# Performance work log

Hardware: AMD Instinct MI355X
Metric: run time of the kernel (lower is better)

Reference implementation:

```python
import jax, jax.numpy as jnp
import numpy as np

N = 100000  # nodes
E = 1600000  # edges
D_IN, D_HID, D_OUT = 128, 128, 64
NEG_SLOPE = 0.2


def gat_conv(x, src, dst, W_src, W_dst, att_src, att_dst, bias, num_nodes):
    # PyG GATConv, heads=1, add_self_loops=False.
    h_src = x @ W_src          # [N, C]
    h_dst = x @ W_dst          # [N, C]
    a_src = (h_src * att_src).sum(-1)   # [N]
    a_dst = (h_dst * att_dst).sum(-1)   # [N]
    logits = jax.nn.leaky_relu(a_src[src] + a_dst[dst], NEG_SLOPE)  # [E]
    # segment softmax over destination neighborhoods
    seg_max = jax.ops.segment_max(logits, dst, num_segments=num_nodes)  # [N]
    e = jnp.exp(logits - seg_max[dst])
    denom = jax.ops.segment_sum(e, dst, num_segments=num_nodes)         # [N]
    alpha = e / (denom[dst] + 1e-16)                                    # [E]
    out = jax.ops.segment_sum(alpha[:, None] * h_src[src], dst, num_segments=num_nodes)  # [N, C]
    return out + bias


def setup_inputs() -> dict:
    key = jax.random.key(0)
    ks = jax.random.split(key, 12)
    x = jax.random.normal(ks[0], (N, D_IN), dtype=jnp.float32)
    edge_index = jax.random.randint(ks[1], (2, E), 0, N, dtype=jnp.int64)
    s1 = 1.0 / np.sqrt(D_IN)
    s2 = 1.0 / np.sqrt(D_HID)
    return {
        "x": x,
        "edge_index": edge_index,
        "W1_src": jax.random.uniform(ks[2], (D_IN, D_HID), jnp.float32, -s1, s1),
        "W1_dst": jax.random.uniform(ks[3], (D_IN, D_HID), jnp.float32, -s1, s1),
        "att1_src": jax.random.uniform(ks[4], (D_HID,), jnp.float32, -s2, s2),
        "att1_dst": jax.random.uniform(ks[5], (D_HID,), jnp.float32, -s2, s2),
        "b1": jnp.zeros((D_HID,), jnp.float32),
        "W2_src": jax.random.uniform(ks[6], (D_HID, D_OUT), jnp.float32, -s2, s2),
        "W2_dst": jax.random.uniform(ks[7], (D_HID, D_OUT), jnp.float32, -s2, s2),
        "att2_src": jax.random.uniform(ks[8], (D_OUT,), jnp.float32, -1.0 / np.sqrt(D_OUT), 1.0 / np.sqrt(D_OUT)),
        "att2_dst": jax.random.uniform(ks[9], (D_OUT,), jnp.float32, -1.0 / np.sqrt(D_OUT), 1.0 / np.sqrt(D_OUT)),
        "b2": jnp.zeros((D_OUT,), jnp.float32),
    }


def reference(x, edge_index, W1_src, W1_dst, att1_src, att1_dst, b1,
              W2_src, W2_dst, att2_src, att2_dst, b2):
    src, dst = edge_index[0], edge_index[1]
    h = gat_conv(x, src, dst, W1_src, W1_dst, att1_src, att1_dst, b1, N)
    h = jax.nn.relu(h)
    out = gat_conv(h, src, dst, W2_src, W2_dst, att2_src, att2_dst, b2, N)
    return out
```

## Files before the change

### kernel.cpp

```cpp
#include <hip/hip_runtime.h>


typedef unsigned long long u64;
typedef float v4f __attribute__((ext_vector_type(4)));
typedef _Float16 v2h __attribute__((ext_vector_type(2)));
typedef __fp16 h8 __attribute__((ext_vector_type(8)));

#define SEL_LO 0x01000504u
#define SEL_HI 0x03020706u

__device__ __forceinline__ void ntstore4(float* p, v4f v) {
    __builtin_nontemporal_store(v, (v4f*)p);
}
__device__ __forceinline__ unsigned h2pack(float a, float b) {
    v2h h;
    h.x = (_Float16)a;
    h.y = (_Float16)b;
    return __builtin_bit_cast(unsigned, h);
}
__device__ __forceinline__ float fdot2u(unsigned u, v2h w, float acc) {
    return __builtin_amdgcn_fdot2(__builtin_bit_cast(v2h, u), w, acc, false);
}
__device__ __forceinline__ v2h pkrtz(float a, float b) {
    return __builtin_bit_cast(v2h, __builtin_amdgcn_cvt_pkrtz(a, b));
}

__device__ void matvec_body(const float* __restrict__ W, const float* __restrict__ a,
                            float* __restrict__ out, int cols, int row) {
    int lane = threadIdx.x & 63;
    float s = 0.f;
    for (int j = lane; j < cols; j += 64) s += W[row * cols + j] * a[j];
#pragma unroll
    for (int o = 32; o; o >>= 1) s += __shfl_xor(s, o, 64);
    if (lane == 0) out[row] = s;
}

template <int C>
__device__ void packw_body(const float* __restrict__ W, uint4* __restrict__ Wp) {
    constexpr int NT = C / 16;
    const int total = 4 * NT * 64;
    for (int e = threadIdx.x; e < total; e += 256) {
        int lane = e & 63;
        int ti = (e >> 6) % NT;
        int t = (e >> 6) / NT;
        int k0 = 32 * t + (lane >> 4) * 8;
        int n = ti * 16 + (lane & 15);
        unsigned u[4];
#pragma unroll
        for (int p = 0; p < 4; ++p)
            u[p] = h2pack(W[(size_t)(k0 + 2 * p) * C + n], W[(size_t)(k0 + 2 * p + 1) * C + n]);
        Wp[e] = make_uint4(u[0], u[1], u[2], u[3]);
    }
}

__global__ __launch_bounds__(256) void setup_kernel(
    const int* __restrict__ dst, int* __restrict__ hist, int E, int nbE,
    const float* __restrict__ W1s, uint4* __restrict__ wp1,
    const float* __restrict__ W2s, uint4* __restrict__ wp2,
    const float* __restrict__ W1d, const float* __restrict__ att1d, float* __restrict__ watt1,
    const float* __restrict__ W2d, const float* __restrict__ att2d, float* __restrict__ watt2) {
    int b = blockIdx.x;
    if (b < nbE) {
        __shared__ int h[256];
        h[threadIdx.x] = 0;
        __syncthreads();
        int base = b * 4096;
        int lim = min(base + 4096, E);
        for (int i = base + threadIdx.x; i < lim; i += 256)
            atomicAdd(&h[__builtin_nontemporal_load(dst + i) >> 9], 1);
        __syncthreads();
        __builtin_nontemporal_store(h[threadIdx.x], hist + b * 256 + threadIdx.x);
    } else if (b == nbE) {
        packw_body<128>(W1s, wp1);
    } else if (b == nbE + 1) {
        packw_body<64>(W2s, wp2);
    } else if (b < nbE + 34) {
        matvec_body(W1d, att1d, watt1, 128, (b - nbE - 2) * 4 + (threadIdx.x >> 6));
    } else {
        matvec_body(W2d, att2d, watt2, 64, (b - nbE - 34) * 4 + (threadIdx.x >> 6));
    }
}

__global__ __launch_bounds__(256) void bscan_kernel(const int* __restrict__ hist, int nbE,
                                                    int* __restrict__ bbase,
                                                    int* __restrict__ gcur,
                                                    int* __restrict__ offs, int N, int E) {
    __shared__ int s[256];
    int t = threadIdx.x;
    int v = 0;
#pragma unroll 4
    for (int b = 0; b < nbE; ++b) v += hist[b * 256 + t];
    s[t] = v;
    __syncthreads();
    for (int o = 1; o < 256; o <<= 1) {
        int u = (t >= o) ? s[t - o] : 0;
        __syncthreads();
        s[t] += u;
        __syncthreads();
    }
    int excl = s[t] - v;
    bbase[t] = excl;
    gcur[t] = excl;
    if (t == 255) { bbase[256] = E; offs[N] = E; }
}

__device__ void scatter_body(const int* __restrict__ src, const int* __restrict__ dst,
                             int* __restrict__ gcur, u64* __restrict__ pairs, int E,
                             int blk, char* smem) {
    int* h = (int*)smem;
    int* sbase = h + 256;
    int* rbase = h + 512;
    u64* buf = (u64*)(smem + 3072);
    const int tid = threadIdx.x;
    h[tid] = 0;
    __syncthreads();
    const int base = blk * 4096;
    const int lim = min(4096, E - base);
    u64 pv[16];
    int rk[16];
    int bk[16];
#pragma unroll 16
    for (int k = 0; k < 16; ++k) {
        int i = base + k * 256 + tid;
        if (i < E) {
            int d = __builtin_nontemporal_load(dst + i);
            int b = d >> 9;
            bk[k] = b;
            pv[k] = ((u64)(unsigned)d << 32) | (unsigned)__builtin_nontemporal_load(src + i);
            rk[k] = atomicAdd(&h[b], 1);
        } else {
            bk[k] = -1;
        }
    }
    __syncthreads();
    const int v = h[tid];
    sbase[tid] = v;
    __syncthreads();
    for (int o = 1; o < 256; o <<= 1) {
        int uu = (tid >= o) ? sbase[tid - o] : 0;
        __syncthreads();
        sbase[tid] += uu;
        __syncthreads();
    }
    const int excl = sbase[tid] - v;
    rbase[tid] = v ? atomicAdd(&gcur[tid], v) : 0;
    __syncthreads();
    sbase[tid] = excl;
    __syncthreads();
#pragma unroll 16
    for (int k = 0; k < 16; ++k)
        if (bk[k] >= 0) buf[sbase[bk[k]] + rk[k]] = pv[k];
    __syncthreads();
    for (int i = tid; i < lim; i += 256) {
        u64 p = buf[i];
        int b = (int)(p >> 41);
        __builtin_nontemporal_store(p, pairs + (size_t)rbase[b] + (i - sbase[b]));
    }
}

__global__ __launch_bounds__(512) void bsort_kernel(const u64* __restrict__ pairs,
                                                    const int* __restrict__ bbase,
                                                    int* __restrict__ offs,
                                                    int* __restrict__ srcs, int N) {
    __shared__ int h[512];
    __shared__ int cur[512];
    const int t = threadIdx.x;
    const int b = blockIdx.x;
    const int beg = bbase[b], end = bbase[b + 1];
    h[t] = 0;
    __syncthreads();
    for (int i = beg + t; i < end; i += 512)
        atomicAdd(&h[(int)(__builtin_nontemporal_load(pairs + i) >> 32) & 511], 1);
    __syncthreads();
    int v = h[t];
    cur[t] = v;
    __syncthreads();
    for (int o = 1; o < 512; o <<= 1) {
        int u = (t >= o) ? cur[t - o] : 0;
        __syncthreads();
        cur[t] += u;
        __syncthreads();
    }
    int pos0 = beg + cur[t] - v;
    __syncthreads();
    cur[t] = pos0;
    int g = (b << 9) + t;
    if (g < N) offs[g] = pos0;
    __syncthreads();
    for (int i = beg + t; i < end; i += 512) {
        u64 p = __builtin_nontemporal_load(pairs + i);
        int local = (int)(p >> 32) & 511;
        int pp = atomicAdd(&cur[local], 1);
        srcs[pp] = (int)(p & 0xffffffffu);
    }
}

template <int C, bool XF16>
__device__ void gemm_body(int blk, const void* __restrict__ Xv, const uint4* __restrict__ Wp,
                          const float* __restrict__ attS, const float* __restrict__ wda,
                          unsigned* __restrict__ H, float* __restrict__ aS,
                          float* __restrict__ aD, int M, _Float16* hsAll) {
    constexpr int NT = C / 16;
    const int tid = threadIdx.x;
    const int w = tid >> 6;
    const int lane = tid & 63;
    const int l15 = lane & 15;
    const int q = lane >> 4;
    const int mb = blk * 64 + w * 16;
    const int m = mb + l15;
    const bool mv = m < M;

    v4f acc[NT];
#pragma unroll
    for (int n = 0; n < NT; ++n) acc[n] = (v4f)(0.f);
    float pd = 0.f;
    uint4 afu[4];

    if constexpr (XF16) {
        const uint4* Xp = (const uint4*)Xv + (size_t)m * 16;
#pragma unroll
        for (int t = 0; t < 4; ++t) {
            uint4 u = make_uint4(0u, 0u, 0u, 0u);
            if (mv) u = Xp[4 * t + q];
            afu[t] = u;
            const float* wdp = wda + 32 * t + 8 * q;
            pd = fdot2u(u.x, pkrtz(wdp[0], wdp[1]), pd);
            pd = fdot2u(u.y, pkrtz(wdp[2], wdp[3]), pd);
            pd = fdot2u(u.z, pkrtz(wdp[4], wdp[5]), pd);
            pd = fdot2u(u.w, pkrtz(wdp[6], wdp[7]), pd);
        }
    } else {
        const float* Xp = (const float*)Xv + (size_t)m * 128;
#pragma unroll
        for (int t = 0; t < 4; ++t) {
            float4 x0 = make_float4(0.f, 0.f, 0.f, 0.f);
            float4 x1 = x0;
            if (mv) {
                x0 = *(const float4*)(Xp + 32 * t + 8 * q);
                x1 = *(const float4*)(Xp + 32 * t + 8 * q + 4);
            }
            const float* wdp = wda + 32 * t + 8 * q;
            pd += x0.x * wdp[0] + x0.y * wdp[1] + x0.z * wdp[2] + x0.w * wdp[3] +
                  x1.x * wdp[4] + x1.y * wdp[5] + x1.z * wdp[6] + x1.w * wdp[7];
            afu[t] = make_uint4(h2pack(x0.x, x0.y), h2pack(x0.z, x0.w),
                                h2pack(x1.x, x1.y), h2pack(x1.z, x1.w));
        }
    }

#pragma unroll
    for (int t = 0; t < 4; ++t) {
        h8 a = __builtin_bit_cast(h8, afu[t]);
        const uint4* wp = Wp + (size_t)t * NT * 64 + lane;
#pragma unroll
        for (int n = 0; n < NT; ++n) {
            h8 b = __builtin_bit_cast(h8, wp[n * 64]);
            acc[n] = __builtin_amdgcn_mfma_f32_16x16x32_f16(a, b, acc[n], 0, 0, 0);
        }
    }

    pd += __shfl_xor(pd, 16, 64);
    pd += __shfl_xor(pd, 32, 64);
    if (q == 0 && mv) aD[m] = pd;

    float as4[4] = {0.f, 0.f, 0.f, 0.f};
#pragma unroll
    for (int n = 0; n < NT; ++n) {
        float av = attS[n * 16 + l15];
#pragma unroll
        for (int r = 0; r < 4; ++r) as4[r] += acc[n][r] * av;
    }
#pragma unroll
    for (int r = 0; r < 4; ++r) {
#pragma unroll
        for (int o = 1; o < 16; o <<= 1) as4[r] += __shfl_xor(as4[r], o, 64);
    }
    if (l15 == 0) {
#pragma unroll
        for (int r = 0; r < 4; ++r) {
            int row = mb + q * 4 + r;
            if (row < M) aS[row] = as4[r];
        }
    }

    _Float16* hp = hsAll + w * (16 * 136);
#pragma unroll
    for (int n = 0; n < NT; ++n)
#pragma unroll
        for (int r = 0; r < 4; ++r)
            hp[(q * 4 + r) * 136 + n * 16 + l15] = (_Float16)acc[n][r];

    constexpr int CH = C / 32;
    if (lane < 16 * CH) {
        int row = lane / CH;
        int ch = lane % CH;
        const uint4* rp = (const uint4*)(hp + row * 136 + ch * 32);
        uint4 v0 = rp[0], v1 = rp[1], v2 = rp[2], v3 = rp[3];
        int gr = mb + row;
        if (gr < M) {
            uint4* op = (uint4*)(H + (size_t)gr * (C / 2)) + ch * 4;
            op[0] = v0; op[1] = v1; op[2] = v2; op[3] = v3;
        }
    }
}

__global__ __launch_bounds__(256) void scatter_gemm_kernel(
    const int* __restrict__ src, const int* __restrict__ dst, int* __restrict__ gcur,
    u64* __restrict__ pairs, int E, int nbS,
    const void* __restrict__ Xv, const uint4* __restrict__ Wp,
    const float* __restrict__ attS, const float* __restrict__ wda,
    unsigned* __restrict__ H, float* __restrict__ aS, float* __restrict__ aD, int M) {
    __shared__ __align__(16) char smem[35840];
    int b = blockIdx.x;
    if (b < nbS) scatter_body(src, dst, gcur, pairs, E, b, smem);
    else gemm_body<128, false>(b - nbS, Xv, Wp, attS, wda, H, aS, aD, M, (_Float16*)smem);
}

template <int C, bool RELU, bool F16OUT, bool NTOUT>
__global__ __launch_bounds__(256) void aggregate_kernel(
    const int* __restrict__ offs, const int* __restrict__ srcs,
    const unsigned* __restrict__ hsrc, const float* __restrict__ aS,
    const float* __restrict__ aD, const float* __restrict__ bias,
    void* __restrict__ outv, int n) {
    const int lane = threadIdx.x & 63;
    const int sl = lane & 31;
    const int hb = lane & 32;
    const int g = (lane >> 4) & 1;
    const int l = lane & 15;
    int node = (int)((blockIdx.x * blockDim.x + threadIdx.x) >> 5);
    if (node >= n) return;

    const int beg = offs[node], end = offs[node + 1];
    const int deg = end - beg;
    const float ad = aD[node];

    constexpr int LW = C / 32;
    constexpr int NA = C / 16;
    float acc[NA];
#pragma unroll
    for (int i = 0; i < NA; ++i) acc[i] = 0.f;

    int sj = 0;
    float u = 0.f;

    auto ldrow = [&](int s, unsigned* r) {
        if constexpr (C == 128) {
            uint4 v = ((const uint4*)(hsrc + ((size_t)s << 6)))[l];
            r[0] = v.x; r[1] = v.y; r[2] = v.z; r[3] = v.w;
        } else {
            uint2 v = ((const uint2*)(hsrc + ((size_t)s << 5)))[l];
            r[0] = v.x; r[1] = v.y;
        }
    };
    auto issue = [&](int j, unsigned (*buf)[LW]) {
        int e0 = hb + j * 8 + g;
        int s0 = __shfl(sj, e0, 64);
        int s1 = __shfl(sj, e0 + 2, 64);
        int s2 = __shfl(sj, e0 + 4, 64);
        int s3 = __shfl(sj, e0 + 6, 64);
        ldrow(s0, buf[0]);
        ldrow(s1, buf[1]);
        ldrow(s2, buf[2]);
        ldrow(s3, buf[3]);
    };
    auto compute = [&](int j, unsigned (*buf)[LW], float inv) {
        int e0 = hb + j * 8 + g;
        float w0 = __shfl(u, e0, 64) * inv, w1 = __shfl(u, e0 + 2, 64) * inv;
        float w2 = __shfl(u, e0 + 4, 64) * inv, w3 = __shfl(u, e0 + 6, 64) * inv;
        v2h w01 = pkrtz(w0, w1);
        v2h w23 = pkrtz(w2, w3);
#pragma unroll
        for (int ii = 0; ii < LW; ++ii) {
            acc[2 * ii] = fdot2u(__builtin_amdgcn_perm(buf[0][ii], buf[1][ii], SEL_LO), w01,
                          fdot2u(__builtin_amdgcn_perm(buf[2][ii], buf[3][ii], SEL_LO), w23, acc[2 * ii]));
            acc[2 * ii + 1] = fdot2u(__builtin_amdgcn_perm(buf[0][ii], buf[1][ii], SEL_HI), w01,
                              fdot2u(__builtin_amdgcn_perm(buf[2][ii], buf[3][ii], SEL_HI), w23, acc[2 * ii + 1]));
        }
    };

    unsigned A0[4][LW], A1[4][LW];

    if (deg <= 32) {
        int i = beg + sl;
        if (i < end) {
            sj = __builtin_nontemporal_load(srcs + i);
            float lg = aS[sj] + ad;
            lg = (lg > 0.f) ? lg : 0.2f * lg;
            u = __expf(lg);
        }
        int jm = (deg + 7) >> 3;
        if (jm > 0) issue(0, A0);
        if (jm > 1) issue(1, A1);
        float s = u;
#pragma unroll
        for (int o = 16; o; o >>= 1) s += __shfl_xor(s, o, 64);
        float inv = 1.f / (s + 1e-16f);
        if (jm > 0) { compute(0, A0, inv); if (jm > 2) issue(2, A0); }
        if (jm > 1) { compute(1, A1, inv); if (jm > 3) issue(3, A1); }
        if (jm > 2) compute(2, A0, inv);
        if (jm > 3) compute(3, A1, inv);
    } else {
        float m = -INFINITY;
        for (int i = beg + sl; i < end; i += 32) {
            float lg = aS[srcs[i]] + ad;
            lg = (lg > 0.f) ? lg : 0.2f * lg;
            m = fmaxf(m, lg);
        }
#pragma unroll
        for (int o = 16; o; o >>= 1) m = fmaxf(m, __shfl_xor(m, o, 64));
        float ssum = 0.f;
        for (int i = beg + sl; i < end; i += 32) {
            float lg = aS[srcs[i]] + ad;
            lg = (lg > 0.f) ? lg : 0.2f * lg;
            ssum += __expf(lg - m);
        }
#pragma unroll
        for (int o = 16; o; o >>= 1) ssum += __shfl_xor(ssum, o, 64);
        float inv = 1.f / (ssum + 1e-16f);
        for (int base = beg; base < end; base += 32) {
            int i = base + sl;
            sj = 0;
            u = 0.f;
            if (i < end) {
                sj = srcs[i];
                float lg = aS[sj] + ad;
                lg = (lg > 0.f) ? lg : 0.2f * lg;
                u = __expf(lg - m);
            }
            int cnt = min(32, end - base);
            int cj = (cnt + 7) >> 3;
            if (cj > 0) issue(0, A0);
            if (cj > 1) issue(1, A1);
            if (cj > 0) { compute(0, A0, inv); if (cj > 2) issue(2, A0); }
            if (cj > 1) { compute(1, A1, inv); if (cj > 3) issue(3, A1); }
            if (cj > 2) compute(2, A0, inv);
            if (cj > 3) compute(3, A1, inv);
        }
    }

#pragma unroll
    for (int i = 0; i < NA; ++i) acc[i] += __shfl_xor(acc[i], 16, 64);

    if (sl < 16) {
        float o[NA];
        const float* bp = bias + l * NA;
#pragma unroll
        for (int i = 0; i < NA; ++i) {
            o[i] = acc[i] + bp[i];
            if (RELU) o[i] = fmaxf(o[i], 0.f);
        }
        if constexpr (F16OUT) {
            unsigned uo[NA / 2];
#pragma unroll
            for (int k = 0; k < NA / 2; ++k) uo[k] = h2pack(o[2 * k], o[2 * k + 1]);
            unsigned* op = (unsigned*)outv + (size_t)node * (C / 2) + l * (NA / 2);
            if constexpr (NA == 8) *(uint4*)op = make_uint4(uo[0], uo[1], uo[2], uo[3]);
            else *(uint2*)op = make_uint2(uo[0], uo[1]);
        } else {
            float* op = (float*)outv + (size_t)node * C + l * NA;
#pragma unroll
            for (int q = 0; q < NA / 4; ++q) {
                v4f ov;
                ov.x = o[q * 4 + 0]; ov.y = o[q * 4 + 1];
                ov.z = o[q * 4 + 2]; ov.w = o[q * 4 + 3];
                if (NTOUT) ntstore4(op + q * 4, ov);
                else *(v4f*)(op + q * 4) = ov;
            }
        }
    }
}

__global__ __launch_bounds__(256) void agg_gemm_kernel(
    const int* __restrict__ offs, const int* __restrict__ srcs,
    const unsigned* __restrict__ hsrc, const float* __restrict__ aS,
    const float* __restrict__ aD, const float* __restrict__ bias,
    const uint4* __restrict__ Wp2, const float* __restrict__ attS2,
    const float* __restrict__ wda2, unsigned* __restrict__ g2h,
    float* __restrict__ aS2, float* __restrict__ aD2, int n) {
    __shared__ __align__(16) _Float16 lds[64 * 136];
    const int tid = threadIdx.x;
    const int lane = tid & 63;
    const int sl = lane & 31;
    const int hb = lane & 32;
    const int g = (lane >> 4) & 1;
    const int l = lane & 15;
    const int nodeBase = blockIdx.x * 64;

    if (nodeBase + 64 > n) {
        for (int i = tid; i < 64 * 136 / 2; i += 256) ((unsigned*)lds)[i] = 0u;
        __syncthreads();
    }

    constexpr int LW = 4;
    constexpr int NA = 8;

    for (int k = 0; k < 8; ++k) {
        const int node = nodeBase + k * 8 + (tid >> 5);
        if (node < n) {
            const int beg = offs[node], end = offs[node + 1];
            const int deg = end - beg;
            const float ad = aD[node];
            float acc[NA];
#pragma unroll
            for (int i = 0; i < NA; ++i) acc[i] = 0.f;
            int sj = 0;
            float u = 0.f;

            auto ldrow = [&](int s, unsigned* r) {
                uint4 v = ((const uint4*)(hsrc + ((size_t)s << 6)))[l];
                r[0] = v.x; r[1] = v.y; r[2] = v.z; r[3] = v.w;
            };
            auto issue = [&](int j, unsigned (*buf)[LW]) {
                int e0 = hb + j * 8 + g;
                int s0 = __shfl(sj, e0, 64);
                int s1 = __shfl(sj, e0 + 2, 64);
                int s2 = __shfl(sj, e0 + 4, 64);
                int s3 = __shfl(sj, e0 + 6, 64);
                ldrow(s0, buf[0]);
                ldrow(s1, buf[1]);
                ldrow(s2, buf[2]);
                ldrow(s3, buf[3]);
            };
            auto compute = [&](int j, unsigned (*buf)[LW], float inv) {
                int e0 = hb + j * 8 + g;
                float w0 = __shfl(u, e0, 64) * inv, w1 = __shfl(u, e0 + 2, 64) * inv;
                float w2 = __shfl(u, e0 + 4, 64) * inv, w3 = __shfl(u, e0 + 6, 64) * inv;
                v2h w01 = pkrtz(w0, w1);
                v2h w23 = pkrtz(w2, w3);
#pragma unroll
                for (int ii = 0; ii < LW; ++ii) {
                    acc[2 * ii] = fdot2u(__builtin_amdgcn_perm(buf[0][ii], buf[1][ii], SEL_LO), w01,
                                  fdot2u(__builtin_amdgcn_perm(buf[2][ii], buf[3][ii], SEL_LO), w23, acc[2 * ii]));
                    acc[2 * ii + 1] = fdot2u(__builtin_amdgcn_perm(buf[0][ii], buf[1][ii], SEL_HI), w01,
                                     fdot2u(__builtin_amdgcn_perm(buf[2][ii], buf[3][ii], SEL_HI), w23, acc[2 * ii + 1]));
                }
            };

            unsigned A0[4][LW], A1[4][LW];

            if (deg <= 32) {
                int i = beg + sl;
                if (i < end) {
                    sj = __builtin_nontemporal_load(srcs + i);
                    float lg = aS[sj] + ad;
                    lg = (lg > 0.f) ? lg : 0.2f * lg;
                    u = __expf(lg);
                }
                int jm = (deg + 7) >> 3;
                if (jm > 0) issue(0, A0);
                if (jm > 1) issue(1, A1);
                float s = u;
#pragma unroll
                for (int o = 16; o; o >>= 1) s += __shfl_xor(s, o, 64);
                float inv = 1.f / (s + 1e-16f);
                if (jm > 0) { compute(0, A0, inv); if (jm > 2) issue(2, A0); }
                if (jm > 1) { compute(1, A1, inv); if (jm > 3) issue(3, A1); }
                if (jm > 2) compute(2, A0, inv);
                if (jm > 3) compute(3, A1, inv);
            } else {
                float m = -INFINITY;
                for (int i = beg + sl; i < end; i += 32) {
                    float lg = aS[srcs[i]] + ad;
                    lg = (lg > 0.f) ? lg : 0.2f * lg;
                    m = fmaxf(m, lg);
                }
#pragma unroll
                for (int o = 16; o; o >>= 1) m = fmaxf(m, __shfl_xor(m, o, 64));
                float ssum = 0.f;
                for (int i = beg + sl; i < end; i += 32) {
                    float lg = aS[srcs[i]] + ad;
                    lg = (lg > 0.f) ? lg : 0.2f * lg;
                    ssum += __expf(lg - m);
                }
#pragma unroll
                for (int o = 16; o; o >>= 1) ssum += __shfl_xor(ssum, o, 64);
                float inv = 1.f / (ssum + 1e-16f);
                for (int base = beg; base < end; base += 32) {
                    int i = base + sl;
                    sj = 0;
                    u = 0.f;
                    if (i < end) {
                        sj = srcs[i];
                        float lg = aS[sj] + ad;
                        lg = (lg > 0.f) ? lg : 0.2f * lg;
                        u = __expf(lg - m);
                    }
                    int cnt = min(32, end - base);
                    int cj = (cnt + 7) >> 3;
                    if (cj > 0) issue(0, A0);
                    if (cj > 1) issue(1, A1);
                    if (cj > 0) { compute(0, A0, inv); if (cj > 2) issue(2, A0); }
                    if (cj > 1) { compute(1, A1, inv); if (cj > 3) issue(3, A1); }
                    if (cj > 2) compute(2, A0, inv);
                    if (cj > 3) compute(3, A1, inv);
                }
            }

#pragma unroll
            for (int i = 0; i < NA; ++i) acc[i] += __shfl_xor(acc[i], 16, 64);

            if (sl < 16) {
                float o[NA];
                const float* bp = bias + l * NA;
#pragma unroll
                for (int i = 0; i < NA; ++i) o[i] = fmaxf(acc[i] + bp[i], 0.f);
                unsigned uo[4];
#pragma unroll
                for (int kk = 0; kk < 4; ++kk) uo[kk] = h2pack(o[2 * kk], o[2 * kk + 1]);
                unsigned* op = (unsigned*)(lds + (size_t)(k * 8 + (tid >> 5)) * 136) + l * 4;
                *(uint4*)op = make_uint4(uo[0], uo[1], uo[2], uo[3]);
            }
        }
    }
    __syncthreads();

    const int w = tid >> 6;
    const int l15 = lane & 15;
    const int q = lane >> 4;
    const int mb = nodeBase + w * 16;
    const int m = mb + l15;
    const bool mv = m < n;
    const _Float16* xrow = lds + (size_t)(w * 16 + l15) * 136;

    v4f acc2[4];
#pragma unroll
    for (int nn = 0; nn < 4; ++nn) acc2[nn] = (v4f)(0.f);
    float pd = 0.f;
    uint4 afu[4];
#pragma unroll
    for (int t = 0; t < 4; ++t) {
        uint4 u = ((const uint4*)xrow)[4 * t + q];
        afu[t] = u;
        const float* wdp = wda2 + 32 * t + 8 * q;
        pd = fdot2u(u.x, pkrtz(wdp[0], wdp[1]), pd);
        pd = fdot2u(u.y, pkrtz(wdp[2], wdp[3]), pd);
        pd = fdot2u(u.z, pkrtz(wdp[4], wdp[5]), pd);
        pd = fdot2u(u.w, pkrtz(wdp[6], wdp[7]), pd);
    }
#pragma unroll
    for (int t = 0; t < 4; ++t) {
        h8 a = __builtin_bit_cast(h8, afu[t]);
        const uint4* wp = Wp2 + (size_t)t * 4 * 64 + lane;
#pragma unroll
        for (int nn = 0; nn < 4; ++nn) {
            h8 b = __builtin_bit_cast(h8, wp[nn * 64]);
            acc2[nn] = __builtin_amdgcn_mfma_f32_16x16x32_f16(a, b, acc2[nn], 0, 0, 0);
        }
    }

    pd += __shfl_xor(pd, 16, 64);
    pd += __shfl_xor(pd, 32, 64);
    if (q == 0 && mv) aD2[m] = pd;

    float as4[4] = {0.f, 0.f, 0.f, 0.f};
#pragma unroll
    for (int nn = 0; nn < 4; ++nn) {
        float av = attS2[nn * 16 + l15];
#pragma unroll
        for (int r = 0; r < 4; ++r) as4[r] += acc2[nn][r] * av;
    }
#pragma unroll
    for (int r = 0; r < 4; ++r) {
#pragma unroll
        for (int o = 1; o < 16; o <<= 1) as4[r] += __shfl_xor(as4[r], o, 64);
    }
    if (l15 == 0) {
#pragma unroll
        for (int r = 0; r < 4; ++r) {
            int row = mb + q * 4 + r;
            if (row < n) aS2[row] = as4[r];
        }
    }

    _Float16* hp = lds + (size_t)w * (16 * 136);
#pragma unroll
    for (int nn = 0; nn < 4; ++nn)
#pragma unroll
        for (int r = 0; r < 4; ++r)
            hp[(q * 4 + r) * 136 + nn * 16 + l15] = (_Float16)acc2[nn][r];

    if (lane < 32) {
        int row = lane >> 1;
        int ch = lane & 1;
        const uint4* rp = (const uint4*)(hp + row * 136 + ch * 32);
        uint4 v0 = rp[0], v1 = rp[1], v2 = rp[2], v3 = rp[3];
        int gr = mb + row;
        if (gr < n) {
            uint4* op = (uint4*)(g2h + (size_t)gr * 32) + ch * 4;
            op[0] = v0; op[1] = v1; op[2] = v2; op[3] = v3;
        }
    }
}

extern "C" void kernel_launch(void* const* d_in, const int* in_sizes, int n_in,
                              void* d_out, int out_size, void* d_ws, size_t ws_size,
                              hipStream_t stream) {
    const float* x     = (const float*)d_in[0];
    const int*   edge  = (const int*)d_in[1];
    const float* W1s   = (const float*)d_in[2];
    const float* W1d   = (const float*)d_in[3];
    const float* att1s = (const float*)d_in[4];
    const float* att1d = (const float*)d_in[5];
    const float* b1    = (const float*)d_in[6];
    const float* W2s   = (const float*)d_in[7];
    const float* W2d   = (const float*)d_in[8];
    const float* att2s = (const float*)d_in[9];
    const float* att2d = (const float*)d_in[10];
    const float* b2    = (const float*)d_in[11];

    const int N = in_sizes[0] / 128;
    const int E = in_sizes[1] / 2;
    const int* srcI = edge;
    const int* dstI = edge + E;

    const int nbE = (E + 4095) / 4096;
    const int nbuckets = (N + 511) >> 9;
    const int gblk = (N + 63) / 64;

    size_t off = 0;
    auto alloc = [&](size_t bytes) {
        void* p = (char*)d_ws + off;
        off += (bytes + 255) & ~(size_t)255;
        return p;
    };
    int*      offs  = (int*)alloc((size_t)(N + 1) * 4);
    int*      srcs  = (int*)alloc((size_t)E * 4);
    int*      hist  = (int*)alloc((size_t)nbE * 256 * 4);
    int*      bbase = (int*)alloc(257 * 4);
    int*      gcur  = (int*)alloc(256 * 4);
    float*    watt1 = (float*)alloc(128 * 4);
    float*    watt2 = (float*)alloc(128 * 4);
    uint4*    wp1   = (uint4*)alloc(4 * 8 * 64 * 16);
    uint4*    wp2   = (uint4*)alloc(4 * 4 * 64 * 16);
    float*    a_s   = (float*)alloc((size_t)N * 4);
    float*    a_d   = (float*)alloc((size_t)N * 4);
    float*    a_s2  = (float*)alloc((size_t)N * 4);
    float*    a_d2  = (float*)alloc((size_t)N * 4);
    unsigned* g1h   = (unsigned*)alloc((size_t)N * 128 * 2);
    unsigned* g2h   = (unsigned*)alloc((size_t)N * 64 * 2);
    u64*      pairs = (u64*)g2h;

    setup_kernel<<<nbE + 66, 256, 0, stream>>>(dstI, hist, E, nbE, W1s, wp1, W2s, wp2,
                                               W1d, att1d, watt1, W2d, att2d, watt2);
    bscan_kernel<<<1, 256, 0, stream>>>(hist, nbE, bbase, gcur, offs, N, E);
    scatter_gemm_kernel<<<nbE + gblk, 256, 0, stream>>>(srcI, dstI, gcur, pairs, E, nbE,
                                                        x, wp1, att1s, watt1, g1h, a_s, a_d, N);
    bsort_kernel<<<nbuckets, 512, 0, stream>>>(pairs, bbase, offs, srcs, N);
    agg_gemm_kernel<<<gblk, 256, 0, stream>>>(offs, srcs, g1h, a_s, a_d, b1,
                                              wp2, att2s, watt2, g2h, a_s2, a_d2, N);
    aggregate_kernel<64, false, false, true><<<(N + 7) / 8, 256, 0, stream>>>(
        offs, srcs, g2h, a_s2, a_d2, b2, d_out, N);
}
```

Baseline: 321.3 us.

## Compact edge pairs to 32-bit, atomic global histogram, widen agg_gemm blocks

Packs each edge into one 32-bit word (local dst index in the high bits, src index in the low 17 bits) instead of a 64-bit pair, which halves the traffic of the scatter and bucket-sort passes. It also cuts scatter LDS use, with a separate byte array holding bucket ids. The per-block histogram array and serial scan are replaced by global atomics into a single 256-entry histogram, cleared by a memset. agg_gemm now runs 512 threads so the aggregation phase covers more rows in parallel, and the extra waves exit before the GEMM phase. The 17-bit src field assumes N is below 131072, and the atomic adds make the bucket totals contend on 256 counters.

```diff
diff --git a/kernel.cpp b/kernel.cpp
--- a/kernel.cpp
+++ b/kernel.cpp
@@ -54,7 +54,7 @@
 }
 
 __global__ __launch_bounds__(256) void setup_kernel(
-    const int* __restrict__ dst, int* __restrict__ hist, int E, int nbE,
+    const int* __restrict__ dst, int* __restrict__ gh, int E, int nbE,
     const float* __restrict__ W1s, uint4* __restrict__ wp1,
     const float* __restrict__ W2s, uint4* __restrict__ wp2,
     const float* __restrict__ W1d, const float* __restrict__ att1d, float* __restrict__ watt1,
@@ -69,7 +69,8 @@
         for (int i = base + threadIdx.x; i < lim; i += 256)
             atomicAdd(&h[__builtin_nontemporal_load(dst + i) >> 9], 1);
         __syncthreads();
-        __builtin_nontemporal_store(h[threadIdx.x], hist + b * 256 + threadIdx.x);
+        int v = h[threadIdx.x];
+        if (v) atomicAdd(&gh[threadIdx.x], v);
     } else if (b == nbE) {
         packw_body<128>(W1s, wp1);
     } else if (b == nbE + 1) {
@@ -81,15 +82,13 @@
     }
 }
 
-__global__ __launch_bounds__(256) void bscan_kernel(const int* __restrict__ hist, int nbE,
+__global__ __launch_bounds__(256) void bscan_kernel(const int* __restrict__ gh,
                                                     int* __restrict__ bbase,
                                                     int* __restrict__ gcur,
                                                     int* __restrict__ offs, int N, int E) {
     __shared__ int s[256];
     int t = threadIdx.x;
-    int v = 0;
-#pragma unroll 4
-    for (int b = 0; b < nbE; ++b) v += hist[b * 256 + t];
+    int v = gh[t];
     s[t] = v;
     __syncthreads();
     for (int o = 1; o < 256; o <<= 1) {
@@ -105,18 +104,19 @@
 }
 
 __device__ void scatter_body(const int* __restrict__ src, const int* __restrict__ dst,
-                             int* __restrict__ gcur, u64* __restrict__ pairs, int E,
+                             int* __restrict__ gcur, unsigned* __restrict__ pairs, int E,
                              int blk, char* smem) {
     int* h = (int*)smem;
     int* sbase = h + 256;
     int* rbase = h + 512;
-    u64* buf = (u64*)(smem + 3072);
+    unsigned* buf = (unsigned*)(smem + 3072);
+    unsigned char* b8 = (unsigned char*)(smem + 19456);
     const int tid = threadIdx.x;
     h[tid] = 0;
     __syncthreads();
     const int base = blk * 4096;
     const int lim = min(4096, E - base);
-    u64 pv[16];
+    unsigned pv[16];
     int rk[16];
     int bk[16];
 #pragma unroll 16
@@ -126,7 +126,8 @@
             int d = __builtin_nontemporal_load(dst + i);
             int b = d >> 9;
             bk[k] = b;
-            pv[k] = ((u64)(unsigned)d << 32) | (unsigned)__builtin_nontemporal_load(src + i);
+            pv[k] = ((unsigned)(d & 511) << 17) |
+                    (unsigned)__builtin_nontemporal_load(src + i);
             rk[k] = atomicAdd(&h[b], 1);
         } else {
             bk[k] = -1;
@@ -149,16 +150,20 @@
     __syncthreads();
 #pragma unroll 16
     for (int k = 0; k < 16; ++k)
-        if (bk[k] >= 0) buf[sbase[bk[k]] + rk[k]] = pv[k];
+        if (bk[k] >= 0) {
+            int pos = sbase[bk[k]] + rk[k];
+            buf[pos] = pv[k];
+            b8[pos] = (unsigned char)bk[k];
+        }
     __syncthreads();
     for (int i = tid; i < lim; i += 256) {
-        u64 p = buf[i];
-        int b = (int)(p >> 41);
+        unsigned p = buf[i];
+        int b = b8[i];
         __builtin_nontemporal_store(p, pairs + (size_t)rbase[b] + (i - sbase[b]));
     }
 }
 
-__global__ __launch_bounds__(512) void bsort_kernel(const u64* __restrict__ pairs,
+__global__ __launch_bounds__(512) void bsort_kernel(const unsigned* __restrict__ pairs,
                                                     const int* __restrict__ bbase,
                                                     int* __restrict__ offs,
                                                     int* __restrict__ srcs, int N) {
@@ -170,7 +175,7 @@
     h[t] = 0;
     __syncthreads();
     for (int i = beg + t; i < end; i += 512)
-        atomicAdd(&h[(int)(__builtin_nontemporal_load(pairs + i) >> 32) & 511], 1);
+        atomicAdd(&h[__builtin_nontemporal_load(pairs + i) >> 17], 1);
     __syncthreads();
     int v = h[t];
     cur[t] = v;
@@ -188,10 +193,10 @@
     if (g < N) offs[g] = pos0;
     __syncthreads();
     for (int i = beg + t; i < end; i += 512) {
-        u64 p = __builtin_nontemporal_load(pairs + i);
-        int local = (int)(p >> 32) & 511;
+        unsigned p = __builtin_nontemporal_load(pairs + i);
+        int local = (int)(p >> 17);
         int pp = atomicAdd(&cur[local], 1);
-        srcs[pp] = (int)(p & 0xffffffffu);
+        srcs[pp] = (int)(p & 0x1FFFFu);
     }
 }
 
@@ -305,11 +310,11 @@
 
 __global__ __launch_bounds__(256) void scatter_gemm_kernel(
     const int* __restrict__ src, const int* __restrict__ dst, int* __restrict__ gcur,
-    u64* __restrict__ pairs, int E, int nbS,
+    unsigned* __restrict__ pairs, int E, int nbS,
     const void* __restrict__ Xv, const uint4* __restrict__ Wp,
     const float* __restrict__ attS, const float* __restrict__ wda,
     unsigned* __restrict__ H, float* __restrict__ aS, float* __restrict__ aD, int M) {
-    __shared__ __align__(16) char smem[35840];
+    __shared__ __align__(16) char smem[23552];
     int b = blockIdx.x;
     if (b < nbS) scatter_body(src, dst, gcur, pairs, E, b, smem);
     else gemm_body<128, false>(b - nbS, Xv, Wp, attS, wda, H, aS, aD, M, (_Float16*)smem);
@@ -469,7 +474,7 @@
     }
 }
 
-__global__ __launch_bounds__(256) void agg_gemm_kernel(
+__global__ __launch_bounds__(512) void agg_gemm_kernel(
     const int* __restrict__ offs, const int* __restrict__ srcs,
     const unsigned* __restrict__ hsrc, const float* __restrict__ aS,
     const float* __restrict__ aD, const float* __restrict__ bias,
@@ -486,15 +491,16 @@
     const int nodeBase = blockIdx.x * 64;
 
     if (nodeBase + 64 > n) {
-        for (int i = tid; i < 64 * 136 / 2; i += 256) ((unsigned*)lds)[i] = 0u;
+        for (int i = tid; i < 64 * 136 / 2; i += 512) ((unsigned*)lds)[i] = 0u;
         __syncthreads();
     }
 
     constexpr int LW = 4;
     constexpr int NA = 8;
 
-    for (int k = 0; k < 8; ++k) {
-        const int node = nodeBase + k * 8 + (tid >> 5);
+    for (int k = 0; k < 4; ++k) {
+        const int row = k * 16 + (tid >> 5);
+        const int node = nodeBase + row;
         if (node < n) {
             const int beg = offs[node], end = offs[node + 1];
             const int deg = end - beg;
@@ -606,7 +612,7 @@
                 unsigned uo[4];
 #pragma unroll
                 for (int kk = 0; kk < 4; ++kk) uo[kk] = h2pack(o[2 * kk], o[2 * kk + 1]);
-                unsigned* op = (unsigned*)(lds + (size_t)(k * 8 + (tid >> 5)) * 136) + l * 4;
+                unsigned* op = (unsigned*)(lds + (size_t)row * 136) + l * 4;
                 *(uint4*)op = make_uint4(uo[0], uo[1], uo[2], uo[3]);
             }
         }
@@ -614,6 +620,7 @@
     __syncthreads();
 
     const int w = tid >> 6;
+    if (w >= 4) return;
     const int l15 = lane & 15;
     const int q = lane >> 4;
     const int mb = nodeBase + w * 16;
@@ -724,7 +731,7 @@
     };
     int*      offs  = (int*)alloc((size_t)(N + 1) * 4);
     int*      srcs  = (int*)alloc((size_t)E * 4);
-    int*      hist  = (int*)alloc((size_t)nbE * 256 * 4);
+    int*      gh    = (int*)alloc(256 * 4);
     int*      bbase = (int*)alloc(257 * 4);
     int*      gcur  = (int*)alloc(256 * 4);
     float*    watt1 = (float*)alloc(128 * 4);
@@ -737,15 +744,16 @@
     float*    a_d2  = (float*)alloc((size_t)N * 4);
     unsigned* g1h   = (unsigned*)alloc((size_t)N * 128 * 2);
     unsigned* g2h   = (unsigned*)alloc((size_t)N * 64 * 2);
-    u64*      pairs = (u64*)g2h;
-
-    setup_kernel<<<nbE + 66, 256, 0, stream>>>(dstI, hist, E, nbE, W1s, wp1, W2s, wp2,
+    unsigned* pairs = (unsigned*)g2h;
+
+    hipMemsetAsync(gh, 0, 256 * 4, stream);
+    setup_kernel<<<nbE + 66, 256, 0, stream>>>(dstI, gh, E, nbE, W1s, wp1, W2s, wp2,
                                                W1d, att1d, watt1, W2d, att2d, watt2);
-    bscan_kernel<<<1, 256, 0, stream>>>(hist, nbE, bbase, gcur, offs, N, E);
+    bscan_kernel<<<1, 256, 0, stream>>>(gh, bbase, gcur, offs, N, E);
     scatter_gemm_kernel<<<nbE + gblk, 256, 0, stream>>>(srcI, dstI, gcur, pairs, E, nbE,
                                                         x, wp1, att1s, watt1, g1h, a_s, a_d, N);
     bsort_kernel<<<nbuckets, 512, 0, stream>>>(pairs, bbase, offs, srcs, N);
-    agg_gemm_kernel<<<gblk, 256, 0, stream>>>(offs, srcs, g1h, a_s, a_d, b1,
+    agg_gemm_kernel<<<gblk, 512, 0, stream>>>(offs, srcs, g1h, a_s, a_d, b1,
                                               wp2, att2s, watt2, g2h, a_s2, a_d2, N);
     aggregate_kernel<64, false, false, true><<<(N + 7) / 8, 256, 0, stream>>>(
         offs, srcs, g2h, a_s2, a_d2, b2, d_out, N);
```

Result: faster. 285.8 us, median of 2 (-11.1%).
